# Kernel tuning notes

Hardware: AMD Instinct MI355X
Metric: run time of the kernel (lower is better)

Reference implementation:

```python
import jax, jax.numpy as jnp
import numpy as np

C = 64; NET = 32; K = 3; G = 4; GC = C // G; P = K * K
STRIDE = 1; PAD = 1; DIL = 1; OFFSET_SCALE = 1.0
BN_EPS = 1e-5; LN_EPS = 1e-6


def conv2d(x, w, b, groups=1, pad=1):
    # x: (N,C,H,W), w: (O, I//groups, kh, kw)
    y = jax.lax.conv_general_dilated(
        x, w, (1, 1), [(pad, pad), (pad, pad)],
        feature_group_count=groups,
        dimension_numbers=('NCHW', 'OIHW', 'NCHW'))
    return y + b[None, :, None, None]


def dcnv3_core(x, offset, mask):
    """Faithful port of dcnv3_core_pytorch (InternImage).
    x: (N,H,W,C) channels-last; offset: (N,H,W,G*P*2); mask: (N,H,W,G*P) (softmaxed).
    grid_sample(bilinear, zeros padding, align_corners=False) done manually."""
    xp = jnp.pad(x, ((0, 0), (PAD, PAD), (PAD, PAD), (0, 0)))
    N, Hin, Win, _ = xp.shape
    Ho, Wo = offset.shape[1], offset.shape[2]
    # reference points in normalized [0,1] coords (x first, y second)
    start = (DIL * (K - 1)) // 2 + 0.5
    ref_x = (start + jnp.arange(Wo, dtype=jnp.float32) * STRIDE) / Win  # (Wo,)
    ref_y = (start + jnp.arange(Ho, dtype=jnp.float32) * STRIDE) / Hin  # (Ho,)
    ref = jnp.stack(jnp.broadcast_arrays(ref_x[None, :], ref_y[:, None]), axis=-1)  # (Ho,Wo,2)
    # dilation grid (kernel tap offsets, torch meshgrid 'ij' flatten order: w-major)
    kv = (jnp.arange(K, dtype=jnp.float32) * DIL - (DIL * (K - 1)) // 2)
    gx, gy = jnp.meshgrid(kv / Win, kv / Hin, indexing='ij')
    grid = jnp.stack([gx, gy], -1).reshape(P, 2)  # (P,2), same for every group
    # sampling locations, normalized: (N,Ho,Wo,G,P,2)
    off = offset.reshape(N, Ho, Wo, G, P, 2) * (OFFSET_SCALE / jnp.array([Win, Hin], jnp.float32))
    loc = ref[None, :, :, None, None, :] + grid[None, None, None, None, :, :] * OFFSET_SCALE + off
    # grid_sample align_corners=False: pixel = loc*size - 0.5  (since g = 2*loc-1)
    px = loc[..., 0] * Win - 0.5
    py = loc[..., 1] * Hin - 0.5
    x0 = jnp.floor(px); y0 = jnp.floor(py)
    ix0 = x0.astype(jnp.int32); iy0 = y0.astype(jnp.int32)
    wx1 = px - x0; wy1 = py - y0; wx0 = 1.0 - wx1; wy0 = 1.0 - wy1
    xg = xp.reshape(N, Hin, Win, G, GC)
    n_idx = jnp.arange(N)[:, None, None, None, None]
    g_idx = jnp.arange(G)[None, None, None, :, None]

    def sample(ix, iy):
        valid = ((ix >= 0) & (ix < Win) & (iy >= 0) & (iy < Hin)).astype(xg.dtype)
        v = xg[n_idx, jnp.clip(iy, 0, Hin - 1), jnp.clip(ix, 0, Win - 1), g_idx]  # (N,Ho,Wo,G,P,GC)
        return v * valid[..., None]

    val = (sample(ix0, iy0) * (wx0 * wy0)[..., None]
           + sample(ix0 + 1, iy0) * (wx1 * wy0)[..., None]
           + sample(ix0, iy0 + 1) * (wx0 * wy1)[..., None]
           + sample(ix0 + 1, iy0 + 1) * (wx1 * wy1)[..., None])
    out = jnp.einsum('nhwgpc,nhwgp->nhwgc', val, mask.reshape(N, Ho, Wo, G, P))
    return out.reshape(N, Ho, Wo, C)


def setup_inputs() -> dict:
    key = jax.random.key(0)
    ks = jax.random.split(key, 16)
    N, H, W = 4, 128, 128
    f = lambda k, shp, s=1.0: jax.random.normal(k, shp, jnp.float32) * s
    return {
        'input_x': f(ks[0], (N, C, H, W)),
        'input_y': f(ks[1], (N, NET, H, W)),
        'enc_w': f(ks[2], (NET, C), 0.05), 'enc_b': jnp.zeros((NET,), jnp.float32),
        'bn_g': jnp.ones((NET,), jnp.float32), 'bn_b': jnp.zeros((NET,), jnp.float32),
        'bn_m': jnp.zeros((NET,), jnp.float32), 'bn_v': jnp.ones((NET,), jnp.float32),
        'gru_wz': f(ks[3], (NET, 2 * NET, 3, 3), 0.05), 'gru_bz': jnp.zeros((NET,), jnp.float32),
        'gru_wr': f(ks[4], (NET, 2 * NET, 3, 3), 0.05), 'gru_br': jnp.zeros((NET,), jnp.float32),
        'gru_wq': f(ks[5], (NET, 2 * NET, 3, 3), 0.05), 'gru_bq': jnp.zeros((NET,), jnp.float32),
        'dw_w': f(ks[6], (C, 1, 3, 3), 0.1), 'dw_b': jnp.zeros((C,), jnp.float32),
        'ln_g': jnp.ones((C,), jnp.float32), 'ln_b': jnp.zeros((C,), jnp.float32),
        'off_w': f(ks[7], (G * P * 2, C), 0.1), 'off_b': f(ks[8], (G * P * 2,), 0.1),
        'mask_w': f(ks[9], (G * P, C), 0.1), 'mask_b': jnp.zeros((G * P,), jnp.float32),
        'inp_w': f(ks[10], (C, C), 0.1), 'inp_b': jnp.zeros((C,), jnp.float32),
        'out_w': f(ks[11], (C, C), 0.1), 'out_b': jnp.zeros((C,), jnp.float32),
    }


def reference(input_x, input_y, enc_w, enc_b, bn_g, bn_b, bn_m, bn_v,
              gru_wz, gru_bz, gru_wr, gru_br, gru_wq, gru_bq,
              dw_w, dw_b, ln_g, ln_b, off_w, off_b, mask_w, mask_b,
              inp_w, inp_b, out_w, out_b):
    N, _, H, W = input_x.shape
    # encoder: 1x1 Conv + BN(eval) + SiLU
    e = jnp.einsum('nchw,oc->nohw', input_x, enc_w) + enc_b[None, :, None, None]
    e = (e - bn_m[None, :, None, None]) * jax.lax.rsqrt(bn_v + BN_EPS)[None, :, None, None]
    e = e * bn_g[None, :, None, None] + bn_b[None, :, None, None]
    x_en = jax.nn.silu(e)
    # ConvGRU: h' = (1-z)*h + z*q
    hx = jnp.concatenate([input_y, x_en], axis=1)
    z = jax.nn.sigmoid(conv2d(hx, gru_wz, gru_bz))
    r = jax.nn.sigmoid(conv2d(hx, gru_wr, gru_br))
    q = jnp.tanh(conv2d(jnp.concatenate([r * input_y, x_en], axis=1), gru_wq, gru_bq))
    h = (1.0 - z) * input_y + z * q  # (N,NET,H,W)
    # channels-last main path
    inp = input_x.transpose(0, 2, 3, 1)  # (N,H,W,C)
    x = inp @ inp_w.T + inp_b
    # depthwise conv on gru state -> LN (channels_last) -> GELU
    y = conv2d(h, dw_w, dw_b, groups=NET).transpose(0, 2, 3, 1)  # (N,H,W,C)
    mu = y.mean(-1, keepdims=True)
    var = ((y - mu) ** 2).mean(-1, keepdims=True)
    y = (y - mu) * jax.lax.rsqrt(var + LN_EPS) * ln_g + ln_b
    y = jax.nn.gelu(y, approximate=False)
    offset = y @ off_w.T + off_b  # (N,H,W,G*P*2)
    m = y @ mask_w.T + mask_b
    m = jax.nn.softmax(m.reshape(N, H, W, G, P), axis=-1).reshape(N, H, W, G * P)
    x = dcnv3_core(x, offset, m)
    x = x @ out_w.T + out_b
    return jax.nn.silu(x.transpose(0, 3, 1, 2)), h
```

## Files before the change

### kernel.cpp

```cpp
#include <hip/hip_runtime.h>
#include <hip/hip_bf16.h>

typedef __hip_bfloat16 bf16;
typedef short short8v __attribute__((ext_vector_type(8)));
typedef short short4v __attribute__((ext_vector_type(4)));
typedef float float4v __attribute__((ext_vector_type(4)));

static __device__ __forceinline__ float b2f(bf16 v){ return __bfloat162float(v); }
static __device__ __forceinline__ bf16 f2b(float v){ return __float2bfloat16(v); }
static __device__ __forceinline__ float bu2f(unsigned short u){ return __uint_as_float(((unsigned)u) << 16); }
static __device__ __forceinline__ short f2bs(float v){ bf16 t = __float2bfloat16(v); return *(short*)&t; }
static __device__ __forceinline__ float ftanh(float x){ return 1.f - 2.f / (1.f + __expf(2.f * x)); }

#define WT 128
#define HWT 16384

#define OFF_WINPB 1024
#define OFF_BZ    20544
#define OFF_BR    39008
#define OFF_BQ    57472
#define OFF_DWP   57504
#define OFF_DWB   58080
#define OFF_LNG   58144
#define OFF_LNB   58208
#define OFF_OMB   65184
#define OFF_WINP  65296
#define OFF_BINP  69392
#define OFF_BOUT  73552
#define NW_TOTAL  73616
#define NBF_ZR    36864
#define NBF_Q     18432
#define NBF_OM    7168
#define NBF_OUT   4096
#define NPREP     (NW_TOTAL + NBF_ZR + NBF_Q + NBF_OM + NBF_OUT)
#define NHALO     2064
#define NTOT      (NPREP + NHALO)
#define NB_PREPB  556

#define B_WZRB  294912
#define B_WQB   368640
#define B_WOMB  405504
#define B_WOUTB 419840
#define B_HXP   428544
#define B_QINP  9081344
#define B_ZBUF  17734144
#define B_XL    428544

__global__ void __launch_bounds__(256) k_stage1(
    const float* __restrict__ enc_w, const float* __restrict__ enc_b,
    const float* __restrict__ bn_g, const float* __restrict__ bn_b,
    const float* __restrict__ bn_m, const float* __restrict__ bn_v,
    const float* __restrict__ gwz, const float* __restrict__ gbz,
    const float* __restrict__ gwr, const float* __restrict__ gbr,
    const float* __restrict__ gwq, const float* __restrict__ gbq,
    const float* __restrict__ dww, const float* __restrict__ dwb,
    const float* __restrict__ lng, const float* __restrict__ lnb,
    const float* __restrict__ offw, const float* __restrict__ offb,
    const float* __restrict__ maskw, const float* __restrict__ maskb,
    const float* __restrict__ inpw, const float* __restrict__ inpb,
    const float* __restrict__ outw, const float* __restrict__ outb,
    float* __restrict__ Wp, bf16* __restrict__ wzrb, bf16* __restrict__ wqb,
    bf16* __restrict__ womb, bf16* __restrict__ woutb,
    bf16* __restrict__ hxp, bf16* __restrict__ qinp,
    const float* __restrict__ X, const float* __restrict__ Y) {
  __shared__ float xls[4096];
  __shared__ float ewls[2048];
  __shared__ float escl[64];
  int tid = threadIdx.x;
  int b = blockIdx.x;

  if (b < NB_PREPB) {
    int i = b * 256 + tid;
    if (i >= NTOT) return;
    if (i >= NPREP) {
      int t = i - NPREP;
      int img = t / 516, r = t % 516;
      int ph, pw;
      if (r < 130) { ph = 0; pw = r; }
      else if (r < 260) { ph = 129; pw = r - 130; }
      else if (r < 388) { ph = r - 260 + 1; pw = 0; }
      else { ph = r - 388 + 1; pw = 129; }
      size_t pb = (((size_t)img * 130 + ph) * 130 + pw) * 64;
      uint4 zz = make_uint4(0, 0, 0, 0);
      #pragma unroll
      for (int k = 0; k < 8; ++k) {
        ((uint4*)(hxp + pb))[k] = zz;
        ((uint4*)(qinp + pb))[k] = zz;
      }
      return;
    }
    if (i >= NW_TOTAL) {
      int d = i - NW_TOTAL;
      if (d < NBF_ZR) {
        int t = d / 9216, rem = d % 9216;
        int kc = rem / 512, rem2 = rem % 512;
        int ln = rem2 >> 3, j = rem2 & 7;
        int n = t * 16 + (ln & 15);
        int cin = (kc & 1) * 32 + ((ln >> 4) << 3) + j;
        int tap = kc >> 1;
        float v = (n < 32) ? gwz[(n*64 + cin)*9 + tap] : gwr[((n-32)*64 + cin)*9 + tap];
        wzrb[d] = f2b(v);
      } else if (d < NBF_ZR + NBF_Q) {
        int d2 = d - NBF_ZR;
        int t = d2 / 9216, rem = d2 % 9216;
        int kc = rem / 512, rem2 = rem % 512;
        int ln = rem2 >> 3, j = rem2 & 7;
        int n = t * 16 + (ln & 15);
        int cin = (kc & 1) * 32 + ((ln >> 4) << 3) + j;
        int tap = kc >> 1;
        wqb[d2] = f2b(gwq[(n*64 + cin)*9 + tap]);
      } else if (d < NBF_ZR + NBF_Q + NBF_OM) {
        int d3 = d - NBF_ZR - NBF_Q;
        int wv = d3 / 1024, rem = d3 % 1024;
        int kc = rem / 512, rem2 = rem % 512;
        int ln = rem2 >> 3, j = rem2 & 7;
        int jcol = wv * 16 + (ln & 15);
        int c = kc * 32 + ((ln >> 4) << 3) + j;
        float v = (jcol < 72) ? offw[jcol*64 + c] : ((jcol < 108) ? maskw[(jcol-72)*64 + c] : 0.f);
        womb[d3] = f2b(v);
      } else {
        int d4 = d - NBF_ZR - NBF_Q - NBF_OM;
        int nt = d4 / 1024, rem = d4 % 1024;
        int kc = rem / 512, rem2 = rem % 512;
        int ln = rem2 >> 3, j = rem2 & 7;
        int o = nt * 16 + (ln & 15);
        int c = kc * 32 + ((ln >> 4) << 3) + j;
        woutb[d4] = f2b(outw[o*64 + c]);
      }
      return;
    }
    float v;
    if (i < 20544) {
      if (i >= OFF_WINPB && i < OFF_WINPB + 2048) {
        int d0 = (i - OFF_WINPB) * 2;
        int nt = d0 >> 10, kc = (d0 >> 9) & 1, lnn = (d0 >> 3) & 63, j0 = d0 & 7;
        int o = nt * 16 + (lnn & 15);
        int c = kc * 32 + ((lnn >> 4) << 3) + j0;
        unsigned lo = (unsigned)(unsigned short)f2bs(inpw[o * 64 + c]);
        unsigned hi = (unsigned)(unsigned short)f2bs(inpw[o * 64 + c + 1]);
        v = __uint_as_float(lo | (hi << 16));
      } else v = 0.f;
    }
    else if (i < 20576) { v = gbz[i - OFF_BZ]; }
    else if (i < 39008) { v = 0.f; }
    else if (i < 39040) { v = gbr[i - OFF_BR]; }
    else if (i < 57472) { v = 0.f; }
    else if (i < 57504) { v = gbq[i - OFF_BQ]; }
    else if (i < 58080) { int d = i - OFF_DWP; int tap = d >> 6, o = d & 63; v = dww[o*9 + tap]; }
    else if (i < 58144) { v = dwb[i - OFF_DWB]; }
    else if (i < 58208) { v = lng[i - OFF_LNG]; }
    else if (i < 58272) { v = lnb[i - OFF_LNB]; }
    else if (i < 65184) { v = 0.f; }
    else if (i < 65292) { int j = i - OFF_OMB; v = (j < 72) ? offb[j] : maskb[j-72]; }
    else if (i < 65296) { v = 0.f; }
    else if (i < 69392) { int d = i - OFF_WINP; int c = d >> 6, o = d & 63; v = inpw[o*64 + c]; }
    else if (i < 69456) { v = inpb[i - OFF_BINP]; }
    else if (i < 73552) { v = 0.f; }
    else { v = outb[i - OFF_BOUT]; }
    Wp[i] = v;
    return;
  }

  int pb2 = b - NB_PREPB;
  int img = pb2 >> 8, h = (pb2 >> 1) & 127, w0 = (pb2 & 1) * 64;
  int px = tid & 63, sect = tid >> 6;
  #pragma unroll
  for (int k = 0; k < 8; ++k) {
    int i2 = k * 256 + tid;
    int c = i2 >> 5, o = i2 & 31;
    ewls[i2] = enc_w[o*64 + c];
  }
  if (tid < 32) {
    float sc = bn_g[tid] * rsqrtf(bn_v[tid] + 1e-5f);
    escl[tid] = sc;
    escl[32 + tid] = (enc_b[tid] - bn_m[tid]) * sc + bn_b[tid];
  }
  int hw = h * WT + w0 + px;
  const float* xp = X + (size_t)img * (64 * HWT) + hw;
  #pragma unroll
  for (int i2 = 0; i2 < 16; ++i2) {
    int c = sect * 16 + i2;
    xls[c * 64 + px] = xp[c * HWT];
  }
  const float* yp = Y + (size_t)img * (32 * HWT) + hw;
  bf16 yv[8];
  #pragma unroll
  for (int i2 = 0; i2 < 8; ++i2) yv[i2] = f2b(yp[(sect * 8 + i2) * HWT]);
  size_t pbb = (((size_t)img * 130 + h + 1) * 130 + (w0 + px + 1)) * 64;
  *(uint4*)(hxp + pbb + sect * 8) = *(const uint4*)yv;
  __syncthreads();
  float aen[8];
  #pragma unroll
  for (int o = 0; o < 8; ++o) aen[o] = 0.f;
  for (int k = 0; k < 64; ++k) {
    float a = xls[k * 64 + px];
    const float* we = ewls + k * 32 + sect * 8;
    #pragma unroll
    for (int o = 0; o < 8; ++o) aen[o] += a * we[o];
  }
  bf16 xe[8];
  #pragma unroll
  for (int o = 0; o < 8; ++o) {
    int oo = sect * 8 + o;
    float e = aen[o] * escl[oo] + escl[32 + oo];
    xe[o] = f2b(e / (1.f + __expf(-e)));
  }
  *(uint4*)(hxp + pbb + 32 + sect * 8) = *(const uint4*)xe;
  *(uint4*)(qinp + pbb + 32 + sect * 8) = *(const uint4*)xe;
}

__global__ void __launch_bounds__(256) k_zr(
    const float* __restrict__ Wp,
    const bf16* __restrict__ hxp, const bf16* __restrict__ wzrb,
    bf16* __restrict__ qinp, bf16* __restrict__ zbuf) {
  __shared__ short zt[32 * 72];
  __shared__ short ryt[64 * 40];
  int tid = threadIdx.x;
  int wv = tid >> 6, ln = tid & 63;
  int quad = ln >> 4, lm = ln & 15;
  int img = blockIdx.z, h = blockIdx.y;
  int x0 = blockIdx.x * 64;
  int p0 = x0 + wv * 16;
  const short* hs = (const short*)hxp;
  const short* ws = (const short*)wzrb;
  size_t rowb = ((size_t)img * 130 + h + 1) * 130;
  const short* ab = hs + (rowb + p0 + lm + 1) * 64 + quad * 8;
  short8v a[18];
  #pragma unroll
  for (int kc = 0; kc < 18; ++kc) {
    const int tap = kc >> 1, cin0 = (kc & 1) * 32;
    const int dd = (tap / 3 - 1) * 130 + (tap % 3 - 1);
    a[kc] = *(const short8v*)(ab + dd * 64 + cin0);
  }
  float4v acc[4];
  #pragma unroll
  for (int t = 0; t < 4; ++t) acc[t] = (float4v){0.f, 0.f, 0.f, 0.f};
  #pragma unroll
  for (int kc = 0; kc < 18; ++kc) {
    #pragma unroll
    for (int t = 0; t < 4; ++t) {
      short8v b = *(const short8v*)(ws + ((t * 18 + kc) * 64 + ln) * 8);
      acc[t] = __builtin_amdgcn_mfma_f32_16x16x32_bf16(a[kc], b, acc[t], 0, 0, 0);
    }
  }
  #pragma unroll
  for (int t = 0; t < 2; ++t) {
    int n = t * 16 + lm;
    float bz = Wp[OFF_BZ + n];
    short zp[4];
    #pragma unroll
    for (int ri = 0; ri < 4; ++ri)
      zp[ri] = f2bs(1.f / (1.f + __expf(-(acc[t][ri] + bz))));
    *(short4v*)(zt + n * 72 + wv * 16 + quad * 4) = *(const short4v*)zp;
  }
  #pragma unroll
  for (int t = 2; t < 4; ++t) {
    int c = (t - 2) * 16 + lm;
    float br = Wp[OFF_BR + c];
    #pragma unroll
    for (int ri = 0; ri < 4; ++ri) {
      int pxl = wv * 16 + quad * 4 + ri;
      float rv = 1.f / (1.f + __expf(-(acc[t][ri] + br)));
      float yy = b2f(hxp[(rowb + x0 + pxl + 1) * 64 + c]);
      ryt[pxl * 40 + c] = f2bs(rv * yy);
    }
  }
  __syncthreads();
  {
    int n2 = tid >> 3, pq = tid & 7;
    short8v z0 = *(const short8v*)(zt + n2 * 72 + pq * 8);
    short* zo = (short*)zbuf + (((size_t)img * 128 + h) * 32 + n2) * 128 + x0 + pq * 8;
    *(short8v*)zo = z0;
  }
  {
    int px = tid >> 2, cq = tid & 3;
    short8v r0 = *(const short8v*)(ryt + px * 40 + cq * 8);
    short* qo = (short*)qinp + (rowb + x0 + px + 1) * 64 + cq * 8;
    *(short8v*)qo = r0;
  }
}

__global__ void __launch_bounds__(256) k_stageB(
    const float* __restrict__ Y, const float* __restrict__ Wp,
    const bf16* __restrict__ qinp, const bf16* __restrict__ wqb,
    const bf16* __restrict__ zbuf, float* __restrict__ outh,
    const float* __restrict__ X, bf16* __restrict__ xl) {
  __shared__ short xs[64 * 72];
  int tid = threadIdx.x;
  int bid = blockIdx.x;
  int xcd = bid & 7, u = bid >> 3;
  int part = u & 1, slot = u >> 1;
  int img = slot >> 5, rem = slot & 31;
  int hh = xcd * 16 + (rem & 15);
  int w0 = (rem >> 4) * 64;
  int wv = tid >> 6, ln = tid & 63, quad = ln >> 4, lm = ln & 15;

  if (part == 0) {
    int p0 = w0 + wv * 16;
    const short* qs = (const short*)qinp;
    const short* ws = (const short*)wqb;
    size_t rowb = ((size_t)img * 130 + hh + 1) * 130;
    const short* ab = qs + (rowb + p0 + lm + 1) * 64 + quad * 8;
    float4v acc0 = (float4v){0.f,0.f,0.f,0.f};
    float4v acc1 = (float4v){0.f,0.f,0.f,0.f};
    #pragma unroll
    for (int kc = 0; kc < 18; ++kc) {
      const int tap = kc >> 1, cin0 = (kc & 1) * 32;
      const int dd = (tap / 3 - 1) * 130 + (tap % 3 - 1);
      short8v a  = *(const short8v*)(ab + dd * 64 + cin0);
      short8v b0 = *(const short8v*)(ws + ((0 * 18 + kc) * 64 + ln) * 8);
      short8v b1 = *(const short8v*)(ws + ((1 * 18 + kc) * 64 + ln) * 8);
      acc0 = __builtin_amdgcn_mfma_f32_16x16x32_bf16(a, b0, acc0, 0, 0, 0);
      acc1 = __builtin_amdgcn_mfma_f32_16x16x32_bf16(a, b1, acc1, 0, 0, 0);
    }
    int px4 = p0 + quad * 4;
    #pragma unroll
    for (int t = 0; t < 2; ++t) {
      float4v acc = t ? acc1 : acc0;
      int n = t * 16 + lm;
      float bq = Wp[OFF_BQ + n];
      size_t gb = ((size_t)img * 32 + n) * HWT + hh * 128 + px4;
      uint2 zz = *(const uint2*)((const short*)zbuf + (((size_t)img * 128 + hh) * 32 + n) * 128 + px4);
      float4 yv = *(const float4*)(Y + gb);
      float z0 = bu2f((unsigned short)(zz.x & 0xFFFFu)), z1 = bu2f((unsigned short)(zz.x >> 16));
      float z2 = bu2f((unsigned short)(zz.y & 0xFFFFu)), z3 = bu2f((unsigned short)(zz.y >> 16));
      float4 o;
      o.x = (1.f - z0) * yv.x + z0 * ftanh(acc[0] + bq);
      o.y = (1.f - z1) * yv.y + z1 * ftanh(acc[1] + bq);
      o.z = (1.f - z2) * yv.z + z2 * ftanh(acc[2] + bq);
      o.w = (1.f - z3) * yv.w + z3 * ftanh(acc[3] + bq);
      *(float4*)(outh + gb) = o;
    }
    return;
  }

  {
    const float* xb = X + (size_t)img * (64 * HWT) + hh * 128 + w0 + wv * 16 + lm;
    short8v a[2];
    #pragma unroll
    for (int kc = 0; kc < 2; ++kc) {
      short tmp[8];
      #pragma unroll
      for (int j = 0; j < 8; ++j)
        tmp[j] = f2bs(xb[(size_t)(kc * 32 + quad * 8 + j) * HWT]);
      a[kc] = *(const short8v*)tmp;
    }
    const short* wib = (const short*)Wp + 2 * OFF_WINPB;
    float4v acc[4];
    #pragma unroll
    for (int nt = 0; nt < 4; ++nt) acc[nt] = (float4v){0.f,0.f,0.f,0.f};
    #pragma unroll
    for (int kc = 0; kc < 2; ++kc) {
      #pragma unroll
      for (int nt = 0; nt < 4; ++nt) {
        short8v b = *(const short8v*)(wib + ((nt * 2 + kc) * 64 + ln) * 8);
        acc[nt] = __builtin_amdgcn_mfma_f32_16x16x32_bf16(a[kc], b, acc[nt], 0, 0, 0);
      }
    }
    #pragma unroll
    for (int nt = 0; nt < 4; ++nt) {
      int o = nt * 16 + lm;
      float bias = Wp[OFF_BINP + o];
      #pragma unroll
      for (int ri = 0; ri < 4; ++ri)
        xs[(wv * 16 + quad * 4 + ri) * 72 + o] = f2bs(acc[nt][ri] + bias);
    }
    __syncthreads();
    int row = tid >> 2, c0 = (tid & 3) * 16;
    short8v v0 = *(const short8v*)(xs + row * 72 + c0);
    short8v v1 = *(const short8v*)(xs + row * 72 + c0 + 8);
    short* op = (short*)xl + ((size_t)img * HWT + hh * 128 + w0 + row) * 64 + c0;
    *(short8v*)op = v0;
    *(short8v*)(op + 8) = v1;
  }
}

#define LDS_PSA  0
#define LDS_PSB  2048
#define LDS_STAT 4096
#define LDS_Y    4608
#define LDS_OM   13824
#define LDS_TOT  28416

__global__ void __launch_bounds__(512) k_mega(
    const float* __restrict__ Wp, const float* __restrict__ hb,
    const bf16* __restrict__ xl, const bf16* __restrict__ womb,
    const bf16* __restrict__ woutb, float* __restrict__ out0) {
  __shared__ char smem[LDS_TOT];
  float* psa  = (float*)(smem + LDS_PSA);
  float* psb  = (float*)(smem + LDS_PSB);
  float* stat = (float*)(smem + LDS_STAT);
  short* yls  = (short*)(smem + LDS_Y);
  short* omls = (short*)(smem + LDS_OM);
  short* vls  = (short*)(smem + LDS_Y);

  int tid = threadIdx.x;
  int bid = blockIdx.x;
  int xcd = bid & 7, slot = bid >> 3;
  int img = slot >> 5;
  int rem = slot & 31;
  int h = xcd * 16 + (rem & 15);
  int w0 = (rem >> 4) * 64;

  int wloc = tid & 63, part = tid >> 6;
  int w = w0 + wloc;
  float yv[8];
  {
    const float* hn = hb + (size_t)img * (32 * HWT);
    #pragma unroll
    for (int i = 0; i < 8; ++i) yv[i] = Wp[OFF_DWB + part*8 + i];
    #pragma unroll
    for (int tap = 0; tap < 9; ++tap) {
      int dy = tap / 3 - 1, dx = tap % 3 - 1;
      int hh = h + dy, ww = w + dx;
      bool ok = ((unsigned)hh < 128u) && ((unsigned)ww < 128u);
      int off = hh * WT + ww;
      #pragma unroll
      for (int j = 0; j < 4; ++j) {
        int cin = part * 4 + j;
        float a = ok ? hn[cin * HWT + off] : 0.f;
        yv[2*j]   += a * Wp[OFF_DWP + tap*64 + part*8 + 2*j];
        yv[2*j+1] += a * Wp[OFF_DWP + tap*64 + part*8 + 2*j+1];
      }
    }
  }
  float lsum = 0.f, lsq = 0.f;
  #pragma unroll
  for (int i = 0; i < 8; ++i) { lsum += yv[i]; lsq += yv[i]*yv[i]; }
  psa[part * 64 + wloc] = lsum;
  psb[part * 64 + wloc] = lsq;
  __syncthreads();
  if (tid < 64) {
    float s = 0.f, q = 0.f;
    #pragma unroll
    for (int p = 0; p < 8; ++p) { s += psa[p*64 + tid]; q += psb[p*64 + tid]; }
    float mu = s * (1.f/64.f);
    float var = q * (1.f/64.f) - mu * mu;
    stat[tid*2] = mu;
    stat[tid*2+1] = rsqrtf(var + 1e-6f);
  }
  __syncthreads();
  {
    float mu = stat[wloc*2], inv = stat[wloc*2+1];
    bf16 tmp[8];
    #pragma unroll
    for (int i = 0; i < 8; ++i) {
      int c = part*8 + i;
      float v = (yv[i] - mu) * inv * Wp[OFF_LNG + c] + Wp[OFF_LNB + c];
      tmp[i] = f2b(0.5f * v * (1.f + erff(v * 0.70710678118654752f)));
    }
    *(short8v*)(yls + wloc*72 + part*8) = *(const short8v*)tmp;
  }
  __syncthreads();

  int wv = tid >> 6, ln = tid & 63, quad = ln >> 4, lm = ln & 15;
  if (wv < 7) {
    const short* wb = (const short*)womb;
    float4v acc[4];
    #pragma unroll
    for (int mt = 0; mt < 4; ++mt) acc[mt] = (float4v){0.f,0.f,0.f,0.f};
    #pragma unroll
    for (int kc = 0; kc < 2; ++kc) {
      short8v b = *(const short8v*)(wb + ((wv * 2 + kc) * 64 + ln) * 8);
      #pragma unroll
      for (int mt = 0; mt < 4; ++mt) {
        short8v a = *(const short8v*)(yls + (mt*16 + lm)*72 + kc*32 + quad*8);
        acc[mt] = __builtin_amdgcn_mfma_f32_16x16x32_bf16(a, b, acc[mt], 0, 0, 0);
      }
    }
    float bias = Wp[OFF_OMB + wv*16 + lm];
    #pragma unroll
    for (int mt = 0; mt < 4; ++mt) {
      #pragma unroll
      for (int ri = 0; ri < 4; ++ri)
        omls[(mt*16 + quad*4 + ri)*114 + wv*16 + lm] = f2bs(acc[mt][ri] + bias);
    }
  }
  __syncthreads();

  {
    int px = tid >> 3, g = (tid >> 1) & 3, half = tid & 1;
    const short* oml = omls + px*114;
    float m[9];
    #pragma unroll
    for (int p = 0; p < 9; ++p) m[p] = bu2f((unsigned short)oml[72 + g*9 + p]);
    float mx = m[0];
    #pragma unroll
    for (int p = 1; p < 9; ++p) mx = fmaxf(mx, m[p]);
    float sum = 0.f;
    #pragma unroll
    for (int p = 0; p < 9; ++p) { m[p] = __expf(m[p] - mx); sum += m[p]; }
    float rs = 1.f / sum;
    int wg = w0 + px;
    const bf16* xn = xl + (size_t)img * (HWT * 64);
    float acc[8];
    #pragma unroll
    for (int i = 0; i < 8; ++i) acc[i] = 0.f;
    for (int p = 0; p < 9; ++p) {
      float bx = (float)(wg + p / 3 - 1);
      float by = (float)(h + p % 3 - 1);
      float ox = bu2f((unsigned short)oml[g*18 + p*2]);
      float oy = bu2f((unsigned short)oml[g*18 + p*2 + 1]);
      float mk = m[p] * rs;
      float pxx = bx + ox, pyy = by + oy;
      float fx = floorf(pxx), fy = floorf(pyy);
      int jx0 = (int)fx, jy0 = (int)fy;
      float wx1 = pxx - fx, wy1 = pyy - fy;
      float wx0 = 1.f - wx1, wy0 = 1.f - wy1;
      int cjx[4] = { jx0, jx0 + 1, jx0, jx0 + 1 };
      int cjy[4] = { jy0, jy0, jy0 + 1, jy0 + 1 };
      float cw[4] = { wx0*wy0, wx1*wy0, wx0*wy1, wx1*wy1 };
      #pragma unroll
      for (int k = 0; k < 4; ++k) {
        if ((unsigned)cjx[k] < 128u && (unsigned)cjy[k] < 128u) {
          float cf = mk * cw[k];
          const bf16* s = xn + (size_t)(cjy[k] * WT + cjx[k]) * 64 + g * 16 + half * 8;
          uint4 u0 = *(const uint4*)(s);
          const unsigned uu[4] = {u0.x,u0.y,u0.z,u0.w};
          #pragma unroll
          for (int q = 0; q < 4; ++q) {
            acc[2*q]     += cf * bu2f((unsigned short)(uu[q] & 0xFFFFu));
            acc[2*q + 1] += cf * bu2f((unsigned short)(uu[q] >> 16));
          }
        }
      }
    }
    bf16 tmp[8];
    #pragma unroll
    for (int i = 0; i < 8; ++i) tmp[i] = f2b(acc[i]);
    *(short8v*)(vls + px*72 + g*16 + half*8) = *(const short8v*)tmp;
  }
  __syncthreads();

  {
    const short* wb = (const short*)woutb;
    #pragma unroll
    for (int s = 0; s < 2; ++s) {
      int tile = wv * 2 + s;
      int nt = tile >> 2, mt = tile & 3;
      float4v acc = (float4v){0.f,0.f,0.f,0.f};
      #pragma unroll
      for (int kc = 0; kc < 2; ++kc) {
        short8v b = *(const short8v*)(wb + ((nt * 2 + kc) * 64 + ln) * 8);
        short8v a = *(const short8v*)(vls + (mt*16 + lm)*72 + kc*32 + quad*8);
        acc = __builtin_amdgcn_mfma_f32_16x16x32_bf16(a, b, acc, 0, 0, 0);
      }
      int ch = nt*16 + lm;
      float bias = Wp[OFF_BOUT + ch];
      float4 v;
      float s0 = acc[0] + bias; v.x = s0 / (1.f + __expf(-s0));
      float s1 = acc[1] + bias; v.y = s1 / (1.f + __expf(-s1));
      float s2 = acc[2] + bias; v.z = s2 / (1.f + __expf(-s2));
      float s3 = acc[3] + bias; v.w = s3 / (1.f + __expf(-s3));
      *(float4*)(out0 + ((size_t)img*64 + ch)*HWT + h*128 + w0 + mt*16 + quad*4) = v;
    }
  }
}

extern "C" void kernel_launch(void* const* d_in, const int* in_sizes, int n_in,
                              void* d_out, int out_size, void* d_ws, size_t ws_size,
                              hipStream_t stream) {
  const float* input_x = (const float*)d_in[0];
  const float* input_y = (const float*)d_in[1];

  float* Wp = (float*)d_ws;
  bf16* WZRB  = (bf16*)((char*)d_ws + B_WZRB);
  bf16* WQB   = (bf16*)((char*)d_ws + B_WQB);
  bf16* WOMB  = (bf16*)((char*)d_ws + B_WOMB);
  bf16* WOUTB = (bf16*)((char*)d_ws + B_WOUTB);
  bf16* HXP   = (bf16*)((char*)d_ws + B_HXP);
  bf16* QINP  = (bf16*)((char*)d_ws + B_QINP);
  bf16* ZBUF  = (bf16*)((char*)d_ws + B_ZBUF);
  bf16* XL    = (bf16*)((char*)d_ws + B_XL);
  float* out0 = (float*)d_out;
  float* outh = (float*)d_out + 4194304;

  k_stage1<<<dim3(NB_PREPB + 1024), dim3(256), 0, stream>>>(
      (const float*)d_in[2], (const float*)d_in[3], (const float*)d_in[4], (const float*)d_in[5],
      (const float*)d_in[6], (const float*)d_in[7], (const float*)d_in[8], (const float*)d_in[9],
      (const float*)d_in[10], (const float*)d_in[11], (const float*)d_in[12], (const float*)d_in[13],
      (const float*)d_in[14], (const float*)d_in[15], (const float*)d_in[16], (const float*)d_in[17],
      (const float*)d_in[18], (const float*)d_in[19], (const float*)d_in[20], (const float*)d_in[21],
      (const float*)d_in[22], (const float*)d_in[23], (const float*)d_in[24], (const float*)d_in[25],
      Wp, WZRB, WQB, WOMB, WOUTB, HXP, QINP, input_x, input_y);
  k_zr<<<dim3(2, 128, 4), dim3(256), 0, stream>>>(Wp, HXP, WZRB, QINP, ZBUF);
  k_stageB<<<dim3(2048), dim3(256), 0, stream>>>(input_y, Wp, QINP, WQB, ZBUF, outh, input_x, XL);
  k_mega<<<dim3(1024), dim3(512), 0, stream>>>(Wp, outh, XL, WOMB, WOUTB, out0);
}
```

Measured before the change: 224.2 us.

## Use MFMA for encoder 1x1 conv and remap blocks to XCD-local rows

The encoder 1x1 convolution in stage1 moves from a scalar FP32 LDS loop to bf16 MFMA instructions. Its results are staged through shared memory so the hxp and qinp stores stay coalesced. Stage1 and k_zr both remap block IDs so that each XCD handles a contiguous band of rows, which is meant to improve L2 locality for the 3x3 halo reads. k_zr also loads its A fragments inside the MFMA loop instead of preloading all 18, which lowers register pressure but may expose load latency.

```diff
diff --git a/kernel.cpp b/kernel.cpp
--- a/kernel.cpp
+++ b/kernel.cpp
@@ -63,9 +63,9 @@
     bf16* __restrict__ womb, bf16* __restrict__ woutb,
     bf16* __restrict__ hxp, bf16* __restrict__ qinp,
     const float* __restrict__ X, const float* __restrict__ Y) {
-  __shared__ float xls[4096];
-  __shared__ float ewls[2048];
   __shared__ float escl[64];
+  __shared__ short ews[2048];
+  __shared__ short es[64 * 40];
   int tid = threadIdx.x;
   int b = blockIdx.x;
 
@@ -162,51 +162,74 @@
   }
 
   int pb2 = b - NB_PREPB;
-  int img = pb2 >> 8, h = (pb2 >> 1) & 127, w0 = (pb2 & 1) * 64;
+  int xcd2 = pb2 & 7, slot2 = pb2 >> 3;
+  int img = slot2 >> 5, rem2 = slot2 & 31;
+  int h = xcd2 * 16 + (rem2 & 15);
+  int w0 = (rem2 >> 4) * 64;
   int px = tid & 63, sect = tid >> 6;
-  #pragma unroll
-  for (int k = 0; k < 8; ++k) {
-    int i2 = k * 256 + tid;
-    int c = i2 >> 5, o = i2 & 31;
-    ewls[i2] = enc_w[o*64 + c];
-  }
   if (tid < 32) {
     float sc = bn_g[tid] * rsqrtf(bn_v[tid] + 1e-5f);
     escl[tid] = sc;
     escl[32 + tid] = (enc_b[tid] - bn_m[tid]) * sc + bn_b[tid];
   }
+  {
+    int frag = tid >> 6, lnx = tid & 63;
+    int ntw = frag >> 1, kcw = frag & 1;
+    int o = ntw * 16 + (lnx & 15);
+    int cb = kcw * 32 + ((lnx >> 4) << 3);
+    short tmpw[8];
+    #pragma unroll
+    for (int j = 0; j < 8; ++j) tmpw[j] = f2bs(enc_w[o * 64 + cb + j]);
+    *(short8v*)(ews + tid * 8) = *(const short8v*)tmpw;
+  }
   int hw = h * WT + w0 + px;
-  const float* xp = X + (size_t)img * (64 * HWT) + hw;
-  #pragma unroll
-  for (int i2 = 0; i2 < 16; ++i2) {
-    int c = sect * 16 + i2;
-    xls[c * 64 + px] = xp[c * HWT];
-  }
   const float* yp = Y + (size_t)img * (32 * HWT) + hw;
   bf16 yv[8];
   #pragma unroll
   for (int i2 = 0; i2 < 8; ++i2) yv[i2] = f2b(yp[(sect * 8 + i2) * HWT]);
   size_t pbb = (((size_t)img * 130 + h + 1) * 130 + (w0 + px + 1)) * 64;
   *(uint4*)(hxp + pbb + sect * 8) = *(const uint4*)yv;
-  __syncthreads();
-  float aen[8];
-  #pragma unroll
-  for (int o = 0; o < 8; ++o) aen[o] = 0.f;
-  for (int k = 0; k < 64; ++k) {
-    float a = xls[k * 64 + px];
-    const float* we = ewls + k * 32 + sect * 8;
-    #pragma unroll
-    for (int o = 0; o < 8; ++o) aen[o] += a * we[o];
-  }
-  bf16 xe[8];
-  #pragma unroll
-  for (int o = 0; o < 8; ++o) {
-    int oo = sect * 8 + o;
-    float e = aen[o] * escl[oo] + escl[32 + oo];
-    xe[o] = f2b(e / (1.f + __expf(-e)));
-  }
-  *(uint4*)(hxp + pbb + 32 + sect * 8) = *(const uint4*)xe;
-  *(uint4*)(qinp + pbb + 32 + sect * 8) = *(const uint4*)xe;
+  int quad = px >> 4, lm = px & 15;
+  const float* xb = X + (size_t)img * (64 * HWT) + h * WT + w0 + sect * 16 + lm;
+  short8v af[2];
+  #pragma unroll
+  for (int kc = 0; kc < 2; ++kc) {
+    short tmp[8];
+    #pragma unroll
+    for (int j = 0; j < 8; ++j)
+      tmp[j] = f2bs(xb[(size_t)(kc * 32 + quad * 8 + j) * HWT]);
+    af[kc] = *(const short8v*)tmp;
+  }
+  __syncthreads();
+  float4v eacc[2];
+  eacc[0] = (float4v){0.f,0.f,0.f,0.f};
+  eacc[1] = (float4v){0.f,0.f,0.f,0.f};
+  #pragma unroll
+  for (int kc = 0; kc < 2; ++kc) {
+    #pragma unroll
+    for (int nt = 0; nt < 2; ++nt) {
+      short8v bb = *(const short8v*)(ews + ((nt * 2 + kc) * 64 + px) * 8);
+      eacc[nt] = __builtin_amdgcn_mfma_f32_16x16x32_bf16(af[kc], bb, eacc[nt], 0, 0, 0);
+    }
+  }
+  #pragma unroll
+  for (int nt = 0; nt < 2; ++nt) {
+    int o = nt * 16 + lm;
+    float sc = escl[o], bi = escl[32 + o];
+    #pragma unroll
+    for (int ri = 0; ri < 4; ++ri) {
+      float e = eacc[nt][ri] * sc + bi;
+      es[(sect * 16 + quad * 4 + ri) * 40 + o] = f2bs(e / (1.f + __expf(-e)));
+    }
+  }
+  __syncthreads();
+  {
+    int row = tid >> 2, c0 = (tid & 3) * 8;
+    short8v v0 = *(const short8v*)(es + row * 40 + c0);
+    size_t ob = (((size_t)img * 130 + h + 1) * 130 + (w0 + row + 1)) * 64 + 32 + c0;
+    *(short8v*)((short*)hxp + ob) = v0;
+    *(short8v*)((short*)qinp + ob) = v0;
+  }
 }
 
 __global__ void __launch_bounds__(256) k_zr(
@@ -218,29 +241,28 @@
   int tid = threadIdx.x;
   int wv = tid >> 6, ln = tid & 63;
   int quad = ln >> 4, lm = ln & 15;
-  int img = blockIdx.z, h = blockIdx.y;
-  int x0 = blockIdx.x * 64;
+  int bid = blockIdx.x;
+  int xcd = bid & 7, slot = bid >> 3;
+  int img = slot >> 5, rem = slot & 31;
+  int h = xcd * 16 + (rem & 15);
+  int x0 = (rem >> 4) * 64;
   int p0 = x0 + wv * 16;
   const short* hs = (const short*)hxp;
   const short* ws = (const short*)wzrb;
   size_t rowb = ((size_t)img * 130 + h + 1) * 130;
   const short* ab = hs + (rowb + p0 + lm + 1) * 64 + quad * 8;
-  short8v a[18];
+  float4v acc[4];
+  #pragma unroll
+  for (int t = 0; t < 4; ++t) acc[t] = (float4v){0.f, 0.f, 0.f, 0.f};
   #pragma unroll
   for (int kc = 0; kc < 18; ++kc) {
     const int tap = kc >> 1, cin0 = (kc & 1) * 32;
     const int dd = (tap / 3 - 1) * 130 + (tap % 3 - 1);
-    a[kc] = *(const short8v*)(ab + dd * 64 + cin0);
-  }
-  float4v acc[4];
-  #pragma unroll
-  for (int t = 0; t < 4; ++t) acc[t] = (float4v){0.f, 0.f, 0.f, 0.f};
-  #pragma unroll
-  for (int kc = 0; kc < 18; ++kc) {
+    short8v a = *(const short8v*)(ab + dd * 64 + cin0);
     #pragma unroll
     for (int t = 0; t < 4; ++t) {
       short8v b = *(const short8v*)(ws + ((t * 18 + kc) * 64 + ln) * 8);
-      acc[t] = __builtin_amdgcn_mfma_f32_16x16x32_bf16(a[kc], b, acc[t], 0, 0, 0);
+      acc[t] = __builtin_amdgcn_mfma_f32_16x16x32_bf16(a, b, acc[t], 0, 0, 0);
     }
   }
   #pragma unroll
@@ -583,7 +605,7 @@
       (const float*)d_in[18], (const float*)d_in[19], (const float*)d_in[20], (const float*)d_in[21],
       (const float*)d_in[22], (const float*)d_in[23], (const float*)d_in[24], (const float*)d_in[25],
       Wp, WZRB, WQB, WOMB, WOUTB, HXP, QINP, input_x, input_y);
-  k_zr<<<dim3(2, 128, 4), dim3(256), 0, stream>>>(Wp, HXP, WZRB, QINP, ZBUF);
+  k_zr<<<dim3(1024), dim3(256), 0, stream>>>(Wp, HXP, WZRB, QINP, ZBUF);
   k_stageB<<<dim3(2048), dim3(256), 0, stream>>>(input_y, Wp, QINP, WQB, ZBUF, outh, input_x, XL);
   k_mega<<<dim3(1024), dim3(512), 0, stream>>>(Wp, outh, XL, WOMB, WOUTB, out0);
 }
```

After: 222.5 us. About the same (-0.7%).
